# Optimization experiments

Hardware: AMD Instinct MI355X
Metric: run time of the kernel (lower is better)

Reference implementation:

```python
import jax, jax.numpy as jnp
import numpy as np

TIER_BITS = [16, 8, 6, 4]


def quantize_ste(x, bits):
    # Fake-quant with straight-through estimator; per-tensor abs-max scale.
    if bits >= 16:
        return x
    max_val = float(2 ** (bits - 1) - 1)
    scale = jnp.maximum(jnp.max(jnp.abs(x)), 1e-8) / max_val
    x_q = jnp.clip(jnp.round(x / scale), -max_val, max_val) * scale
    return x + jax.lax.stop_gradient(x_q - x)


def setup_inputs() -> dict:
    key = jax.random.key(0)
    ks = jax.random.split(key, 6)
    dim = 1024
    sizes = [256, 2048 - 256, 16384 - 2048, 50257 - 16384]  # tier row counts
    tws = [jax.random.normal(ks[i], (sizes[i], dim), dtype=jnp.float32) * 0.02 for i in range(4)]
    input_ids = jax.random.randint(ks[4], (8, 2048), 0, 50257, dtype=jnp.int64)
    return {
        "input_ids": input_ids,
        "tw0": tws[0], "tw1": tws[1], "tw2": tws[2], "tw3": tws[3],
        "ts0": jnp.ones((1, dim), jnp.float32) * 0.1,
        "ts1": jnp.ones((1, dim), jnp.float32) * 0.1,
        "ts2": jnp.ones((1, dim), jnp.float32) * 0.1,
        "ts3": jnp.ones((1, dim), jnp.float32) * 0.1,
    }


def reference(input_ids, tw0, tw1, tw2, tw3, ts0, ts1, ts2, ts3):
    tws = [tw0, tw1, tw2, tw3]
    tss = [ts0, ts1, ts2, ts3]
    # Rebuild the full fake-quantized vocab table (same math as the torch module),
    # then gather the requested rows.
    table = jnp.concatenate(
        [quantize_ste(tws[i] * tss[i], TIER_BITS[i]) for i in range(4)], axis=0
    )  # [vocab, dim]
    return jnp.take(table, input_ids, axis=0)  # [B, S, dim]
```

## Files before the change

### kernel.cpp

```cpp
#include <hip/hip_runtime.h>

#define DIM 1024
#define D4  (DIM / 4)

typedef float vfloat4 __attribute__((ext_vector_type(4)));

__global__ __launch_bounds__(256) void absmax3_kernel(
    const float4* __restrict__ tw1, const float4* __restrict__ ts1, long n1,
    const float4* __restrict__ tw2, const float4* __restrict__ ts2, long n2,
    const float4* __restrict__ tw3, const float4* __restrict__ ts3, long n3,
    int b1, int b2, unsigned* __restrict__ amax)
{
    __shared__ float smax[4];
    int bid = blockIdx.x;
    const float4 *tw, *ts; long n4; int blo, bhi; unsigned* out;
    if (bid < b1)      { tw = tw1; ts = ts1; n4 = n1; blo = 0;  bhi = b1;        out = amax + 0; }
    else if (bid < b2) { tw = tw2; ts = ts2; n4 = n2; blo = b1; bhi = b2;        out = amax + 1; }
    else               { tw = tw3; ts = ts3; n4 = n3; blo = b2; bhi = gridDim.x; out = amax + 2; }

    long idx    = (long)(bid - blo) * blockDim.x + threadIdx.x;
    long stride = (long)(bhi - blo) * blockDim.x;
    float m = 0.0f;
    for (long i = idx; i < n4; i += stride) {
        float4 v = tw[i];
        float4 s = ts[i & (D4 - 1)];
        m = fmaxf(m, fmaxf(fmaxf(fabsf(v.x * s.x), fabsf(v.y * s.y)),
                           fmaxf(fabsf(v.z * s.z), fabsf(v.w * s.w))));
    }
    for (int off = 32; off > 0; off >>= 1)
        m = fmaxf(m, __shfl_down(m, off));
    if ((threadIdx.x & 63) == 0) smax[threadIdx.x >> 6] = m;
    __syncthreads();
    if (threadIdx.x == 0) {
        float bm = fmaxf(fmaxf(smax[0], smax[1]), fmaxf(smax[2], smax[3]));
        atomicMax(out, __float_as_uint(bm));
    }
}

__global__ __launch_bounds__(256) void gather_quant_kernel(
    const int* __restrict__ ids,
    const float* __restrict__ tw0, const float* __restrict__ tw1,
    const float* __restrict__ tw2, const float* __restrict__ tw3,
    const float* __restrict__ ts0, const float* __restrict__ ts1,
    const float* __restrict__ ts2, const float* __restrict__ ts3,
    const unsigned* __restrict__ amax, float* __restrict__ out)
{
    int token = blockIdx.x;
    int id = ids[token];

    const float* tw; const float* ts;
    float maxval = 0.f; unsigned am = 0; bool quant = true;
    if (id < 256)        { tw = tw0 + (long)id * DIM;           ts = ts0; quant = false; }
    else if (id < 2048)  { tw = tw1 + (long)(id - 256) * DIM;   ts = ts1; maxval = 127.f; am = amax[0]; }
    else if (id < 16384) { tw = tw2 + (long)(id - 2048) * DIM;  ts = ts2; maxval = 31.f;  am = amax[1]; }
    else                 { tw = tw3 + (long)(id - 16384) * DIM; ts = ts3; maxval = 7.f;   am = amax[2]; }

    int t = threadIdx.x;
    float4 v = ((const float4*)tw)[t];
    float4 s = ((const float4*)ts)[t];
    vfloat4 x;
    x.x = v.x * s.x; x.y = v.y * s.y; x.z = v.z * s.z; x.w = v.w * s.w;

    if (quant) {
        float scale = fmaxf(__uint_as_float(am), 1e-8f) / maxval;
        x.x = fminf(fmaxf(rintf(x.x / scale), -maxval), maxval) * scale;
        x.y = fminf(fmaxf(rintf(x.y / scale), -maxval), maxval) * scale;
        x.z = fminf(fmaxf(rintf(x.z / scale), -maxval), maxval) * scale;
        x.w = fminf(fmaxf(rintf(x.w / scale), -maxval), maxval) * scale;
    }
    __builtin_nontemporal_store(x, (vfloat4*)(out + (long)token * DIM) + t);
}

extern "C" void kernel_launch(void* const* d_in, const int* in_sizes, int n_in,
                              void* d_out, int out_size, void* d_ws, size_t ws_size,
                              hipStream_t stream) {
    const int*   ids = (const int*)d_in[0];
    const float* tw0 = (const float*)d_in[1];
    const float* tw1 = (const float*)d_in[2];
    const float* tw2 = (const float*)d_in[3];
    const float* tw3 = (const float*)d_in[4];
    const float* ts0 = (const float*)d_in[5];
    const float* ts1 = (const float*)d_in[6];
    const float* ts2 = (const float*)d_in[7];
    const float* ts3 = (const float*)d_in[8];
    float* out = (float*)d_out;

    unsigned* amax = (unsigned*)d_ws;
    (void)hipMemsetAsync(d_ws, 0, 3 * sizeof(unsigned), stream);

    long n1 = (long)in_sizes[2] / 4;
    long n2 = (long)in_sizes[3] / 4;
    long n3 = (long)in_sizes[4] / 4;
    long N  = n1 + n2 + n3;

    const int G = 2048;
    int b1 = (int)((n1 * G + N - 1) / N); if (b1 < 1) b1 = 1;
    int b2 = b1 + (int)((n2 * G) / N);    if (b2 <= b1) b2 = b1 + 1;
    if (b2 >= G) b2 = G - 1;

    absmax3_kernel<<<G, 256, 0, stream>>>(
        (const float4*)tw1, (const float4*)ts1, n1,
        (const float4*)tw2, (const float4*)ts2, n2,
        (const float4*)tw3, (const float4*)ts3, n3,
        b1, b2, amax);

    int n_tokens = in_sizes[0];
    gather_quant_kernel<<<n_tokens, 256, 0, stream>>>(
        ids, tw0, tw1, tw2, tw3, ts0, ts1, ts2, ts3, amax, out);
}
```

Baseline: 298.9 us.

## Unroll absmax with hoisted scale multiply and map one wave per gathered token

The abs-max reduction now keeps four independent float4 running maxima and issues four loads per loop iteration, so more memory requests are in flight. Because the grid stride is a multiple of the row width, each thread always sees the same column, so the per-column scale is applied once after the loop as max|v|·|s| instead of per element. That removes the scale loads and multiplies from the hot loop. The gather kernel now handles four tokens per block, one wavefront each, with four vector loads per lane. The scale-hoisting relies on the stride-alignment invariant holding.

After: 290.7 us. 2.8% less time.

```diff
diff --git a/kernel.cpp b/kernel.cpp
--- a/kernel.cpp
+++ b/kernel.cpp
@@ -5,7 +5,13 @@
 
 typedef float vfloat4 __attribute__((ext_vector_type(4)));
 
-__global__ __launch_bounds__(256) void absmax3_kernel(
+static __device__ __forceinline__ float4 abs_max4(float4 m, float4 v) {
+    m.x = fmaxf(m.x, fabsf(v.x)); m.y = fmaxf(m.y, fabsf(v.y));
+    m.z = fmaxf(m.z, fabsf(v.z)); m.w = fmaxf(m.w, fabsf(v.w));
+    return m;
+}
+
+__global__ __launch_bounds__(256, 8) void absmax3_kernel(
     const float4* __restrict__ tw1, const float4* __restrict__ ts1, long n1,
     const float4* __restrict__ tw2, const float4* __restrict__ ts2, long n2,
     const float4* __restrict__ tw3, const float4* __restrict__ ts3, long n3,
@@ -20,13 +26,24 @@
 
     long idx    = (long)(bid - blo) * blockDim.x + threadIdx.x;
     long stride = (long)(bhi - blo) * blockDim.x;
-    float m = 0.0f;
-    for (long i = idx; i < n4; i += stride) {
-        float4 v = tw[i];
-        float4 s = ts[i & (D4 - 1)];
-        m = fmaxf(m, fmaxf(fmaxf(fabsf(v.x * s.x), fabsf(v.y * s.y)),
-                           fmaxf(fabsf(v.z * s.z), fabsf(v.w * s.w))));
+
+    float4 ma = {0,0,0,0}, mb = {0,0,0,0}, mc = {0,0,0,0}, md = {0,0,0,0};
+    long i = idx;
+    for (; i + 3 * stride < n4; i += 4 * stride) {
+        float4 a = tw[i];
+        float4 b = tw[i + stride];
+        float4 c = tw[i + 2 * stride];
+        float4 d = tw[i + 3 * stride];
+        ma = abs_max4(ma, a); mb = abs_max4(mb, b);
+        mc = abs_max4(mc, c); md = abs_max4(md, d);
     }
+    for (; i < n4; i += stride) ma = abs_max4(ma, tw[i]);
+
+    ma = abs_max4(ma, mb); mc = abs_max4(mc, md); ma = abs_max4(ma, mc);
+    float4 s = ts[idx & (D4 - 1)];
+    float m = fmaxf(fmaxf(ma.x * fabsf(s.x), ma.y * fabsf(s.y)),
+                    fmaxf(ma.z * fabsf(s.z), ma.w * fabsf(s.w)));
+
     for (int off = 32; off > 0; off >>= 1)
         m = fmaxf(m, __shfl_down(m, off));
     if ((threadIdx.x & 63) == 0) smax[threadIdx.x >> 6] = m;
@@ -38,37 +55,52 @@
 }
 
 __global__ __launch_bounds__(256) void gather_quant_kernel(
-    const int* __restrict__ ids,
+    const int* __restrict__ ids, int n_tokens,
     const float* __restrict__ tw0, const float* __restrict__ tw1,
     const float* __restrict__ tw2, const float* __restrict__ tw3,
     const float* __restrict__ ts0, const float* __restrict__ ts1,
     const float* __restrict__ ts2, const float* __restrict__ ts3,
     const unsigned* __restrict__ amax, float* __restrict__ out)
 {
-    int token = blockIdx.x;
+    int sub  = threadIdx.x >> 6;
+    int lane = threadIdx.x & 63;
+    int token = blockIdx.x * 4 + sub;
+    if (token >= n_tokens) return;
     int id = ids[token];
 
     const float* tw; const float* ts;
-    float maxval = 0.f; unsigned am = 0; bool quant = true;
+    float maxval = 1.f; unsigned am = 0; bool quant = true;
     if (id < 256)        { tw = tw0 + (long)id * DIM;           ts = ts0; quant = false; }
     else if (id < 2048)  { tw = tw1 + (long)(id - 256) * DIM;   ts = ts1; maxval = 127.f; am = amax[0]; }
     else if (id < 16384) { tw = tw2 + (long)(id - 2048) * DIM;  ts = ts2; maxval = 31.f;  am = amax[1]; }
     else                 { tw = tw3 + (long)(id - 16384) * DIM; ts = ts3; maxval = 7.f;   am = amax[2]; }
 
-    int t = threadIdx.x;
-    float4 v = ((const float4*)tw)[t];
-    float4 s = ((const float4*)ts)[t];
-    vfloat4 x;
-    x.x = v.x * s.x; x.y = v.y * s.y; x.z = v.z * s.z; x.w = v.w * s.w;
+    const float4* twv = (const float4*)tw;
+    const float4* tsv = (const float4*)ts;
 
-    if (quant) {
-        float scale = fmaxf(__uint_as_float(am), 1e-8f) / maxval;
-        x.x = fminf(fmaxf(rintf(x.x / scale), -maxval), maxval) * scale;
-        x.y = fminf(fmaxf(rintf(x.y / scale), -maxval), maxval) * scale;
-        x.z = fminf(fmaxf(rintf(x.z / scale), -maxval), maxval) * scale;
-        x.w = fminf(fmaxf(rintf(x.w / scale), -maxval), maxval) * scale;
+    float4 v0 = twv[lane +   0], v1 = twv[lane +  64];
+    float4 v2 = twv[lane + 128], v3 = twv[lane + 192];
+    float4 s0 = tsv[lane +   0], s1 = tsv[lane +  64];
+    float4 s2 = tsv[lane + 128], s3 = tsv[lane + 192];
+
+    float scale = fmaxf(__uint_as_float(am), 1e-8f) / maxval;
+
+    float4 vv[4] = {v0, v1, v2, v3};
+    float4 ss[4] = {s0, s1, s2, s3};
+    float* outp = out + (long)token * DIM;
+    #pragma unroll
+    for (int j = 0; j < 4; ++j) {
+        vfloat4 x;
+        x.x = vv[j].x * ss[j].x; x.y = vv[j].y * ss[j].y;
+        x.z = vv[j].z * ss[j].z; x.w = vv[j].w * ss[j].w;
+        if (quant) {
+            x.x = fminf(fmaxf(rintf(x.x / scale), -maxval), maxval) * scale;
+            x.y = fminf(fmaxf(rintf(x.y / scale), -maxval), maxval) * scale;
+            x.z = fminf(fmaxf(rintf(x.z / scale), -maxval), maxval) * scale;
+            x.w = fminf(fmaxf(rintf(x.w / scale), -maxval), maxval) * scale;
+        }
+        __builtin_nontemporal_store(x, (vfloat4*)outp + lane + 64 * j);
     }
-    __builtin_nontemporal_store(x, (vfloat4*)(out + (long)token * DIM) + t);
 }
 
 extern "C" void kernel_launch(void* const* d_in, const int* in_sizes, int n_in,
@@ -105,6 +137,6 @@
         b1, b2, amax);
 
     int n_tokens = in_sizes[0];
-    gather_quant_kernel<<<n_tokens, 256, 0, stream>>>(
-        ids, tw0, tw1, tw2, tw3, ts0, ts1, ts2, ts3, amax, out);
+    gather_quant_kernel<<<(n_tokens + 3) / 4, 256, 0, stream>>>(
+        ids, n_tokens, tw0, tw1, tw2, tw3, ts0, ts1, ts2, ts3, amax, out);
 }
```
